# Optimization experiments

Hardware: AMD Instinct MI355X
Metric: run time of the kernel (lower is better)

## Reference

```python
import jax, jax.numpy as jnp
import numpy as np

B, T, C, H, L, V = 4, 1024, 1024, 16, 6, 32000
D = C // H
STD = 0.02


def setup_inputs() -> dict:
    key = jax.random.key(0)
    ks = jax.random.split(key, 12)
    return {
        "idx": jax.random.randint(ks[0], (B, T), 0, V),
        "tok_emb": jax.random.normal(ks[1], (V, C), jnp.float32) * STD,
        "pos_emb": jax.random.normal(ks[2], (T, C), jnp.float32) * STD,
        "qkv_w": jax.random.normal(ks[3], (L, C, 3 * C), jnp.float32) * STD,
        "attn_out_w": jax.random.normal(ks[4], (L, C, C), jnp.float32) * STD,
        "attn_out_b": jnp.zeros((L, C), jnp.float32),
        "fc1_w": jax.random.normal(ks[5], (L, C, 4 * C), jnp.float32) * STD,
        "fc1_b": jnp.zeros((L, 4 * C), jnp.float32),
        "fc2_w": jax.random.normal(ks[6], (L, 4 * C, C), jnp.float32) * STD,
        "fc2_b": jnp.zeros((L, C), jnp.float32),
        "ln1_w": jnp.ones((L, C), jnp.float32),
        "ln1_b": jnp.zeros((L, C), jnp.float32),
        "ln2_w": jnp.ones((L, C), jnp.float32),
        "ln2_b": jnp.zeros((L, C), jnp.float32),
        "lnf_w": jnp.ones((C,), jnp.float32),
        "lnf_b": jnp.zeros((C,), jnp.float32),
        "head_w": jax.random.normal(ks[7], (C, V), jnp.float32) * STD,
    }


def layernorm(x, w, b, eps=1e-5):
    mu = jnp.mean(x, axis=-1, keepdims=True)
    var = jnp.var(x, axis=-1, keepdims=True)
    return (x - mu) * jax.lax.rsqrt(var + eps) * w + b


def attention(x, qkv_w, out_w, out_b, causal_mask):
    # x: (B,T,C)
    qkv = jnp.einsum("btc,cf->btf", x, qkv_w)  # (B,T,3C)
    q, k, v = jnp.split(qkv, 3, axis=-1)
    q = q.reshape(B, T, H, D).transpose(0, 2, 1, 3)  # (B,H,T,D)
    k = k.reshape(B, T, H, D).transpose(0, 2, 1, 3)
    v = v.reshape(B, T, H, D).transpose(0, 2, 1, 3)
    scores = jnp.einsum("bhqd,bhkd->bhqk", q, k) / np.sqrt(D).astype(np.float32)
    scores = jnp.where(causal_mask, scores, -jnp.inf)
    w = jax.nn.softmax(scores, axis=-1)
    out = jnp.einsum("bhqk,bhkd->bhqd", w, v)  # (B,H,T,D)
    out = out.transpose(0, 2, 1, 3).reshape(B, T, C)
    return jnp.einsum("btc,cd->btd", out, out_w) + out_b


def reference(idx, tok_emb, pos_emb, qkv_w, attn_out_w, attn_out_b,
              fc1_w, fc1_b, fc2_w, fc2_b, ln1_w, ln1_b, ln2_w, ln2_b,
              lnf_w, lnf_b, head_w):
    causal_mask = jnp.tril(jnp.ones((T, T), dtype=bool))[None, None]  # (1,1,T,T)
    x = tok_emb[idx] + pos_emb[jnp.arange(T)][None]  # (B,T,C)
    for l in range(L):
        h = layernorm(x, ln1_w[l], ln1_b[l])
        x = x + attention(h, qkv_w[l], attn_out_w[l], attn_out_b[l], causal_mask)
        h = layernorm(x, ln2_w[l], ln2_b[l])
        h = jax.nn.relu(jnp.einsum("btc,cf->btf", h, fc1_w[l]) + fc1_b[l])
        x = x + jnp.einsum("btf,fc->btc", h, fc2_w[l]) + fc2_b[l]
    x = layernorm(x, lnf_w, lnf_b)
    logits = jnp.einsum("btc,cv->btv", x, head_w)  # (B,T,V)
    return logits
```

## Files before the change

### kernel.cpp

```cpp
#include <hip/hip_runtime.h>
#include <cstdint>
#include <cstddef>

typedef __bf16 bf16_t;
typedef __bf16 bf16x8 __attribute__((ext_vector_type(8)));
typedef float f32x4 __attribute__((ext_vector_type(4)));

#define B_ 4
#define T_ 1024
#define C_ 1024
#define H_ 16
#define L_ 6
#define V_ 32000
#define M_ (B_ * T_)

__global__ __launch_bounds__(256) void k_embed(const int* __restrict__ idx,
                                               const float* __restrict__ tok,
                                               const float* __restrict__ pos,
                                               float* __restrict__ x) {
  int row = blockIdx.x;
  int t = row & (T_ - 1);
  int id = idx[row];
  int c = threadIdx.x * 4;
  f32x4 a = *(const f32x4*)(tok + (size_t)id * C_ + c);
  f32x4 p = *(const f32x4*)(pos + (size_t)t * C_ + c);
  *(f32x4*)(x + (size_t)row * C_ + c) = a + p;
}

__global__ __launch_bounds__(256) void k_ln(const float* __restrict__ x,
                                            const float* __restrict__ w,
                                            const float* __restrict__ b,
                                            bf16_t* __restrict__ out) {
  __shared__ float red[8];
  int row = blockIdx.x;
  int tid = threadIdx.x;
  const float* xr = x + (size_t)row * C_;
  f32x4 v = *(const f32x4*)(xr + tid * 4);
  float s = v[0] + v[1] + v[2] + v[3];
  float q = v[0] * v[0] + v[1] * v[1] + v[2] * v[2] + v[3] * v[3];
#pragma unroll
  for (int off = 32; off; off >>= 1) {
    s += __shfl_xor(s, off);
    q += __shfl_xor(q, off);
  }
  int wid = tid >> 6;
  if ((tid & 63) == 0) { red[wid * 2] = s; red[wid * 2 + 1] = q; }
  __syncthreads();
  s = red[0] + red[2] + red[4] + red[6];
  q = red[1] + red[3] + red[5] + red[7];
  float mu = s * (1.f / C_);
  float var = q * (1.f / C_) - mu * mu;
  float rstd = rsqrtf(var + 1e-5f);
  f32x4 wv = *(const f32x4*)(w + tid * 4);
  f32x4 bv = *(const f32x4*)(b + tid * 4);
  bf16_t* o = out + (size_t)row * C_ + tid * 4;
#pragma unroll
  for (int j = 0; j < 4; j++) o[j] = (bf16_t)((v[j] - mu) * rstd * wv[j] + bv[j]);
}

__global__ __launch_bounds__(256) void k_transpose_bf16(const float* __restrict__ in,
                                                        bf16_t* __restrict__ out,
                                                        int K, int N) {
  __shared__ float tile[32][33];
  int n0 = blockIdx.x * 32, k0 = blockIdx.y * 32;
  int tid = threadIdx.x;
  int cr = tid >> 5, cc = tid & 31;
#pragma unroll
  for (int it = 0; it < 4; it++) {
    int r = it * 8 + cr;
    tile[r][cc] = in[(size_t)(k0 + r) * N + n0 + cc];
  }
  __syncthreads();
#pragma unroll
  for (int it = 0; it < 4; it++) {
    int r = it * 8 + cr;
    out[(size_t)(n0 + r) * K + k0 + cc] = (bf16_t)tile[cc][r];
  }
}

__global__ __launch_bounds__(256) void k_reshape_qk(const bf16_t* __restrict__ qkv,
                                                    bf16_t* __restrict__ qh,
                                                    bf16_t* __restrict__ kh) {
  int g = blockIdx.x * 256 + threadIdx.x;
  int d = g & 63;
  int t = (g >> 6) & (T_ - 1);
  int h = (g >> 16) & (H_ - 1);
  int b = g >> 20;
  size_t src = ((size_t)(b * T_ + t)) * (3 * C_) + h * 64 + d;
  qh[g] = (bf16_t)((float)qkv[src] * 0.125f);
  kh[g] = qkv[src + C_];
}

__global__ __launch_bounds__(256) void k_vtrans(const bf16_t* __restrict__ qkv,
                                                bf16_t* __restrict__ vT) {
  __shared__ bf16_t tile[64][65];
  int bh = blockIdx.x;
  int t0 = blockIdx.y * 64;
  int tid = threadIdx.x;
  int c = tid & 63, rr = tid >> 6;
  int b = bh >> 4, h = bh & (H_ - 1);
  const bf16_t* src = qkv + ((size_t)(b * T_ + t0)) * (3 * C_) + 2 * C_ + h * 64;
#pragma unroll
  for (int it = 0; it < 16; it++) {
    int r = it * 4 + rr;
    tile[r][c] = src[(size_t)r * (3 * C_) + c];
  }
  __syncthreads();
  bf16_t* dst = vT + (size_t)bh * 64 * T_ + t0;
#pragma unroll
  for (int it = 0; it < 16; it++) {
    int dr = it * 4 + rr;
    dst[(size_t)dr * T_ + c] = tile[c][dr];
  }
}

__global__ __launch_bounds__(256) void k_attn(const bf16_t* __restrict__ qh,
                                              const bf16_t* __restrict__ kh,
                                              const bf16_t* __restrict__ vT,
                                              bf16_t* __restrict__ outb) {
  __shared__ bf16_t p_lds[4][16 * 32];
  int tid = threadIdx.x, lane = tid & 63, wid = tid >> 6;
  int bh = blockIdx.x;
  int b = bh >> 4, h = bh & (H_ - 1);
  int qbase = blockIdx.y * 64 + wid * 16;
  const bf16_t* qp = qh + ((size_t)bh * T_ + qbase) * 64;
  const bf16_t* kp = kh + (size_t)bh * T_ * 64;
  const bf16_t* vp = vT + (size_t)bh * 64 * T_;
  int r = lane & 15, g = lane >> 4;

  bf16x8 qf0 = *(const bf16x8*)(qp + r * 64 + g * 8);
  bf16x8 qf1 = *(const bf16x8*)(qp + r * 64 + 32 + g * 8);

  f32x4 o[4];
  float m[4], l[4];
#pragma unroll
  for (int j = 0; j < 4; j++) { m[j] = -1e30f; l[j] = 0.f; o[j] = (f32x4){0.f, 0.f, 0.f, 0.f}; }

  int kv_end = qbase + 16;
  for (int jb = 0; jb < kv_end; jb += 32) {
    f32x4 s0 = (f32x4){0.f, 0.f, 0.f, 0.f};
    f32x4 s1 = (f32x4){0.f, 0.f, 0.f, 0.f};
    const bf16_t* kb0 = kp + (size_t)(jb + r) * 64 + g * 8;
    const bf16_t* kb1 = kb0 + 16 * 64;
    s0 = __builtin_amdgcn_mfma_f32_16x16x32_bf16(qf0, *(const bf16x8*)(kb0), s0, 0, 0, 0);
    s0 = __builtin_amdgcn_mfma_f32_16x16x32_bf16(qf1, *(const bf16x8*)(kb0 + 32), s0, 0, 0, 0);
    s1 = __builtin_amdgcn_mfma_f32_16x16x32_bf16(qf0, *(const bf16x8*)(kb1), s1, 0, 0, 0);
    s1 = __builtin_amdgcn_mfma_f32_16x16x32_bf16(qf1, *(const bf16x8*)(kb1 + 32), s1, 0, 0, 0);

    float p0[4], p1[4], fac[4];
#pragma unroll
    for (int j = 0; j < 4; j++) {
      int rowg = qbase + g * 4 + j;
      float v0 = s0[j], v1 = s1[j];
      if (jb + r > rowg) v0 = -1e30f;
      if (jb + 16 + r > rowg) v1 = -1e30f;
      float t = fmaxf(v0, v1);
      t = fmaxf(t, __shfl_xor(t, 1));
      t = fmaxf(t, __shfl_xor(t, 2));
      t = fmaxf(t, __shfl_xor(t, 4));
      t = fmaxf(t, __shfl_xor(t, 8));
      float nm = fmaxf(m[j], t);
      p0[j] = __expf(v0 - nm);
      p1[j] = __expf(v1 - nm);
      float f = __expf(m[j] - nm);
      float ts = p0[j] + p1[j];
      ts += __shfl_xor(ts, 1);
      ts += __shfl_xor(ts, 2);
      ts += __shfl_xor(ts, 4);
      ts += __shfl_xor(ts, 8);
      l[j] = l[j] * f + ts;
      m[j] = nm;
      fac[j] = f;
    }
    f32x4 fv = (f32x4){fac[0], fac[1], fac[2], fac[3]};
#pragma unroll
    for (int d = 0; d < 4; d++) o[d] *= fv;

    bf16_t* pl = p_lds[wid];
#pragma unroll
    for (int j = 0; j < 4; j++) {
      pl[(g * 4 + j) * 32 + r] = (bf16_t)p0[j];
      pl[(g * 4 + j) * 32 + 16 + r] = (bf16_t)p1[j];
    }
    bf16x8 pa = *(const bf16x8*)(pl + r * 32 + g * 8);
#pragma unroll
    for (int d = 0; d < 4; d++) {
      const bf16_t* vf = vp + (size_t)(d * 16 + r) * T_ + jb + g * 8;
      o[d] = __builtin_amdgcn_mfma_f32_16x16x32_bf16(pa, *(const bf16x8*)(vf), o[d], 0, 0, 0);
    }
  }

#pragma unroll
  for (int d = 0; d < 4; d++) {
#pragma unroll
    for (int j = 0; j < 4; j++) {
      float val = o[d][j] / l[j];
      outb[((size_t)(b * T_ + qbase + g * 4 + j)) * C_ + h * 64 + d * 16 + r] = (bf16_t)val;
    }
  }
}

__device__ __forceinline__ void gld_lds16(const bf16_t* g, bf16_t* l) {
  __builtin_amdgcn_global_load_lds((const __attribute__((address_space(1))) void*)g,
                                   (__attribute__((address_space(3))) void*)l, 16, 0, 0);
}

template <int OUTBF, int HASB, int HASRELU, int HASRES>
__global__ __launch_bounds__(256) void k_gemm(const bf16_t* __restrict__ A,
                                              const bf16_t* __restrict__ Bt,
                                              const float* __restrict__ bias,
                                              const float* resid,
                                              void* Cout, int M, int N, int K) {
  __shared__ bf16_t As[2][128 * 32];
  __shared__ bf16_t Bs[2][128 * 32];
  int tid = threadIdx.x;
  int lane = tid & 63, wid = tid >> 6;
  size_t rowBase = (size_t)blockIdx.y * 128;
  size_t colBase = (size_t)blockIdx.x * 128;

  const bf16_t* gA = A + (rowBase + (tid >> 2)) * (size_t)K + (tid & 3) * 8;
  const bf16_t* gB = Bt + (colBase + (tid >> 2)) * (size_t)K + (tid & 3) * 8;
  const size_t gStep64 = (size_t)64 * K;

  f32x4 acc[4][4];
#pragma unroll
  for (int i = 0; i < 4; i++)
#pragma unroll
    for (int j = 0; j < 4; j++) acc[i][j] = (f32x4){0.f, 0.f, 0.f, 0.f};

  int NK = K >> 5;
  {
    bf16_t* la = &As[0][0] + wid * 512;
    bf16_t* lb = &Bs[0][0] + wid * 512;
    gld_lds16(gA, la);            gld_lds16(gA + gStep64, la + 2048);
    gld_lds16(gB, lb);            gld_lds16(gB + gStep64, lb + 2048);
  }

  int wr = (wid >> 1) * 64, wc = (wid & 1) * 64;
  int r15 = lane & 15, g4 = lane >> 4;

  for (int kt = 0; kt < NK; kt++) {
    int buf = kt & 1;
    __syncthreads();
    if (kt + 1 < NK) {
      const bf16_t* ga = gA + (size_t)(kt + 1) * 32;
      const bf16_t* gb = gB + (size_t)(kt + 1) * 32;
      bf16_t* la = &As[buf ^ 1][0] + wid * 512;
      bf16_t* lb = &Bs[buf ^ 1][0] + wid * 512;
      gld_lds16(ga, la);          gld_lds16(ga + gStep64, la + 2048);
      gld_lds16(gb, lb);          gld_lds16(gb + gStep64, lb + 2048);
    }
    const bf16_t* as = &As[buf][0] + (wr + r15) * 32 + g4 * 8;
    const bf16_t* bs = &Bs[buf][0] + (wc + r15) * 32 + g4 * 8;
    bf16x8 af[4], bfr[4];
#pragma unroll
    for (int i = 0; i < 4; i++) af[i] = *(const bf16x8*)(as + i * 16 * 32);
#pragma unroll
    for (int i = 0; i < 4; i++) bfr[i] = *(const bf16x8*)(bs + i * 16 * 32);
#pragma unroll
    for (int i = 0; i < 4; i++)
#pragma unroll
      for (int j = 0; j < 4; j++)
        acc[i][j] = __builtin_amdgcn_mfma_f32_16x16x32_bf16(af[i], bfr[j], acc[i][j], 0, 0, 0);
  }

#pragma unroll
  for (int i = 0; i < 4; i++) {
    size_t row0 = rowBase + wr + i * 16 + g4 * 4;
#pragma unroll
    for (int j = 0; j < 4; j++) {
      size_t col = colBase + wc + j * 16 + r15;
      float bi = HASB ? bias[col] : 0.f;
#pragma unroll
      for (int q = 0; q < 4; q++) {
        size_t row = row0 + q;
        float v = acc[i][j][q] + bi;
        if (HASRELU) v = fmaxf(v, 0.f);
        if (HASRES) v += resid[row * (size_t)N + col];
        if (OUTBF)
          ((bf16_t*)Cout)[row * (size_t)N + col] = (bf16_t)v;
        else
          ((float*)Cout)[row * (size_t)N + col] = v;
      }
    }
  }
}

extern "C" void kernel_launch(void* const* d_in, const int* in_sizes, int n_in,
                              void* d_out, int out_size, void* d_ws, size_t ws_size,
                              hipStream_t stream) {
  (void)in_sizes; (void)n_in; (void)out_size; (void)ws_size;
  const int* idx = (const int*)d_in[0];
  const float* tok_emb = (const float*)d_in[1];
  const float* pos_emb = (const float*)d_in[2];
  const float* qkv_w = (const float*)d_in[3];
  const float* attn_out_w = (const float*)d_in[4];
  const float* attn_out_b = (const float*)d_in[5];
  const float* fc1_w = (const float*)d_in[6];
  const float* fc1_b = (const float*)d_in[7];
  const float* fc2_w = (const float*)d_in[8];
  const float* fc2_b = (const float*)d_in[9];
  const float* ln1_w = (const float*)d_in[10];
  const float* ln1_b = (const float*)d_in[11];
  const float* ln2_w = (const float*)d_in[12];
  const float* ln2_b = (const float*)d_in[13];
  const float* lnf_w = (const float*)d_in[14];
  const float* lnf_b = (const float*)d_in[15];
  const float* head_w = (const float*)d_in[16];
  float* out = (float*)d_out;

  char* wsp = (char*)d_ws;
  auto alloc = [&](size_t bytes) {
    char* p = wsp;
    wsp += (bytes + 255) & ~(size_t)255;
    return p;
  };
  float* x      = (float*)alloc((size_t)M_ * C_ * 4);
  bf16_t* hbuf  = (bf16_t*)alloc((size_t)M_ * C_ * 2);
  bf16_t* qkvb  = (bf16_t*)alloc((size_t)M_ * 3 * C_ * 2);
  bf16_t* qhb   = (bf16_t*)alloc((size_t)M_ * C_ * 2);
  bf16_t* khb   = (bf16_t*)alloc((size_t)M_ * C_ * 2);
  bf16_t* vTb   = (bf16_t*)alloc((size_t)M_ * C_ * 2);
  bf16_t* attnb = (bf16_t*)alloc((size_t)M_ * C_ * 2);
  bf16_t* midb  = (bf16_t*)alloc((size_t)M_ * 4 * C_ * 2);
  bf16_t* qkvwT = (bf16_t*)alloc((size_t)3 * C_ * C_ * 2);
  bf16_t* owT   = (bf16_t*)alloc((size_t)C_ * C_ * 2);
  bf16_t* fc1wT = (bf16_t*)alloc((size_t)4 * C_ * C_ * 2);
  bf16_t* fc2wT = (bf16_t*)alloc((size_t)4 * C_ * C_ * 2);
  bf16_t* headwT= (bf16_t*)alloc((size_t)C_ * V_ * 2);

  k_embed<<<M_, 256, 0, stream>>>(idx, tok_emb, pos_emb, x);
  k_transpose_bf16<<<dim3(V_ / 32, C_ / 32), 256, 0, stream>>>(head_w, headwT, C_, V_);

  for (int l = 0; l < L_; l++) {
    k_transpose_bf16<<<dim3(3 * C_ / 32, C_ / 32), 256, 0, stream>>>(
        qkv_w + (size_t)l * C_ * 3 * C_, qkvwT, C_, 3 * C_);
    k_transpose_bf16<<<dim3(C_ / 32, C_ / 32), 256, 0, stream>>>(
        attn_out_w + (size_t)l * C_ * C_, owT, C_, C_);
    k_transpose_bf16<<<dim3(4 * C_ / 32, C_ / 32), 256, 0, stream>>>(
        fc1_w + (size_t)l * C_ * 4 * C_, fc1wT, C_, 4 * C_);
    k_transpose_bf16<<<dim3(C_ / 32, 4 * C_ / 32), 256, 0, stream>>>(
        fc2_w + (size_t)l * 4 * C_ * C_, fc2wT, 4 * C_, C_);

    k_ln<<<M_, 256, 0, stream>>>(x, ln1_w + l * C_, ln1_b + l * C_, hbuf);
    k_gemm<1, 0, 0, 0><<<dim3(3 * C_ / 128, M_ / 128), 256, 0, stream>>>(
        hbuf, qkvwT, nullptr, nullptr, qkvb, M_, 3 * C_, C_);
    k_reshape_qk<<<(M_ * C_) / 256, 256, 0, stream>>>(qkvb, qhb, khb);
    k_vtrans<<<dim3(B_ * H_, T_ / 64), 256, 0, stream>>>(qkvb, vTb);
    k_attn<<<dim3(B_ * H_, T_ / 64), 256, 0, stream>>>(qhb, khb, vTb, attnb);
    k_gemm<0, 1, 0, 1><<<dim3(C_ / 128, M_ / 128), 256, 0, stream>>>(
        attnb, owT, attn_out_b + l * C_, x, x, M_, C_, C_);

    k_ln<<<M_, 256, 0, stream>>>(x, ln2_w + l * C_, ln2_b + l * C_, hbuf);
    k_gemm<1, 1, 1, 0><<<dim3(4 * C_ / 128, M_ / 128), 256, 0, stream>>>(
        hbuf, fc1wT, fc1_b + (size_t)l * 4 * C_, nullptr, midb, M_, 4 * C_, C_);
    k_gemm<0, 1, 0, 1><<<dim3(C_ / 128, M_ / 128), 256, 0, stream>>>(
        midb, fc2wT, fc2_b + l * C_, x, x, M_, C_, 4 * C_);
  }

  k_ln<<<M_, 256, 0, stream>>>(x, lnf_w, lnf_b, hbuf);
  k_gemm<0, 0, 0, 0><<<dim3(V_ / 128, M_ / 128), 256, 0, stream>>>(
      hbuf, headwT, nullptr, nullptr, out, M_, V_, C_);
}
```

Baseline: 2.454 ms.

## Add 256x256 tiled GEMM with swizzled LDS, XCD-aware block mapping and interleaved prefetch

Adds a new 512-thread GEMM kernel that computes 256x256 output tiles with a K-step of 64. It stages A and B into XOR-swizzled LDS through direct global-to-LDS loads, splits each K-step into four MFMA quadrants with next-tile prefetch placed between them, and maps blocks to XCDs with a swizzle to improve L2 locality. The QKV, FC1 and LM-head GEMMs switch to this kernel to get more operand reuse per byte loaded and better overlap of loads with MFMA. The trade-offs are more registers and LDS per block (64 KB), fewer blocks for occupancy, and inline asm waitcnt and barrier scheduling that is fragile.

```diff
diff --git a/kernel.cpp b/kernel.cpp
--- a/kernel.cpp
+++ b/kernel.cpp
@@ -5,6 +5,7 @@
 typedef __bf16 bf16_t;
 typedef __bf16 bf16x8 __attribute__((ext_vector_type(8)));
 typedef float f32x4 __attribute__((ext_vector_type(4)));
+typedef int i32x4 __attribute__((ext_vector_type(4)));
 
 #define B_ 4
 #define T_ 1024
@@ -204,6 +205,14 @@
   __builtin_amdgcn_global_load_lds((const __attribute__((address_space(1))) void*)g,
                                    (__attribute__((address_space(3))) void*)l, 16, 0, 0);
 }
+__device__ __forceinline__ bf16x8 lds_rd128(uint32_t addr) {
+  i32x4 d;
+  asm volatile("ds_read_b128 %0, %1" : "=v"(d) : "v"(addr));
+  return __builtin_bit_cast(bf16x8, d);
+}
+#define BAR_() __builtin_amdgcn_s_barrier()
+#define SCHED0_() __builtin_amdgcn_sched_barrier(0)
+#define WLG0_() do { asm volatile("s_waitcnt lgkmcnt(0)" ::: "memory"); SCHED0_(); } while (0)
 
 template <int OUTBF, int HASB, int HASRELU, int HASRES>
 __global__ __launch_bounds__(256) void k_gemm(const bf16_t* __restrict__ A,
@@ -275,6 +284,146 @@
       for (int q = 0; q < 4; q++) {
         size_t row = row0 + q;
         float v = acc[i][j][q] + bi;
+        if (HASRELU) v = fmaxf(v, 0.f);
+        if (HASRES) v += resid[row * (size_t)N + col];
+        if (OUTBF)
+          ((bf16_t*)Cout)[row * (size_t)N + col] = (bf16_t)v;
+        else
+          ((float*)Cout)[row * (size_t)N + col] = v;
+      }
+    }
+  }
+}
+
+#define STAGE_(q, tk, bufv)                                                           \
+  do {                                                                                \
+    const bf16_t* _ga = A + (size_t)(rowBase + (q)*64 + srow) * (size_t)K +           \
+                        (size_t)(tk)*64 + scol;                                       \
+    const bf16_t* _gb = Bt + (size_t)(colBase + (q)*64 + srow) * (size_t)K +          \
+                        (size_t)(tk)*64 + scol;                                       \
+    gld_lds16(_ga, AsF + (bufv)*16384 + (q)*4096 + w * 512);                          \
+    gld_lds16(_gb, BsF + (bufv)*16384 + (q)*4096 + w * 512);                          \
+  } while (0)
+
+#define LDA_(mh, bufv)                                                                \
+  do {                                                                                \
+    uint32_t _ab = aRd + (uint32_t)(bufv)*32768u + (mh)*8192u;                        \
+    _Pragma("unroll") for (int _m = 0; _m < 4; _m++)                                  \
+        _Pragma("unroll") for (int _k = 0; _k < 2; _k++)                              \
+            af[_m][_k] = lds_rd128(_ab + _m * 2048 + _k * 64);                        \
+  } while (0)
+
+#define LDB_(nh, bufv)                                                                \
+  do {                                                                                \
+    uint32_t _bb = bRd + (uint32_t)(bufv)*32768u + (nh)*4096u;                        \
+    _Pragma("unroll") for (int _n = 0; _n < 2; _n++)                                  \
+        _Pragma("unroll") for (int _k = 0; _k < 2; _k++)                              \
+            bfr[_n][_k] = lds_rd128(_bb + _n * 2048 + _k * 64);                       \
+  } while (0)
+
+#define MFQ_(mh, nh)                                                                  \
+  do {                                                                                \
+    __builtin_amdgcn_s_setprio(1);                                                    \
+    _Pragma("unroll") for (int _m = 0; _m < 4; _m++)                                  \
+        _Pragma("unroll") for (int _n = 0; _n < 2; _n++)                              \
+            _Pragma("unroll") for (int _k = 0; _k < 2; _k++)                          \
+                acc[(mh)*4 + _m][(nh)*2 + _n] = __builtin_amdgcn_mfma_f32_16x16x32_bf16( \
+                    af[_m][_k], bfr[_n][_k], acc[(mh)*4 + _m][(nh)*2 + _n], 0, 0, 0); \
+    __builtin_amdgcn_s_setprio(0);                                                    \
+  } while (0)
+
+template <int OUTBF, int HASB, int HASRELU, int HASRES>
+__global__ __launch_bounds__(512, 2) void k_gemm256(const bf16_t* __restrict__ A,
+                                                    const bf16_t* __restrict__ Bt,
+                                                    const float* __restrict__ bias,
+                                                    const float* resid,
+                                                    void* Cout, int M, int N, int K) {
+  __shared__ bf16_t As[2][256][64];
+  __shared__ bf16_t Bs[2][256][64];
+  bf16_t* AsF = &As[0][0][0];
+  bf16_t* BsF = &Bs[0][0][0];
+  const uint32_t asb = (uint32_t)(uintptr_t)AsF;
+  const uint32_t bsb = (uint32_t)(uintptr_t)BsF;
+
+  int tid = threadIdx.x, lane = tid & 63, w = tid >> 6;
+  int wr = w >> 2, wc = w & 3;
+  int r15 = lane & 15, g4 = lane >> 4;
+
+  int nwg = (int)gridDim.x;
+  int bid = (int)blockIdx.x;
+  int xcd = bid & 7, loc = bid >> 3;
+  int q8 = nwg >> 3, r8 = nwg & 7;
+  int swz = (xcd < r8) ? xcd * (q8 + 1) + loc : r8 * (q8 + 1) + (xcd - r8) * q8 + loc;
+  int nY = M >> 8;
+  int by = swz % nY, bx = swz / nY;
+  int rowBase = by * 256, colBase = bx * 256;
+
+  int srow = w * 8 + (lane >> 3);
+  int scol = ((lane & 7) * 8) ^ ((lane & 32) >> 1);
+
+  uint32_t xm = (uint32_t)((r15 & 4) << 3);
+  uint32_t aRd = (asb + (uint32_t)(((wr * 128 + r15) * 64 + g4 * 8) * 2)) ^ xm;
+  uint32_t bRd = (bsb + (uint32_t)(((wc * 64 + r15) * 64 + g4 * 8) * 2)) ^ xm;
+
+  f32x4 acc[8][4];
+#pragma unroll
+  for (int i = 0; i < 8; i++)
+#pragma unroll
+    for (int j = 0; j < 4; j++) acc[i][j] = (f32x4){0.f, 0.f, 0.f, 0.f};
+
+  bf16x8 af[4][2], bfr[2][2];
+
+#pragma unroll
+  for (int q = 0; q < 4; q++) STAGE_(q, 0, 0);
+
+  int NT = K >> 6;
+  for (int kt = 0; kt < NT; ++kt) {
+    int buf = kt & 1;
+    bool pf = (kt + 1 < NT);
+    if (pf) {
+      STAGE_(0, kt + 1, buf ^ 1);
+      asm volatile("s_waitcnt vmcnt(2)" ::: "memory");
+    } else {
+      asm volatile("s_waitcnt vmcnt(0)" ::: "memory");
+    }
+    BAR_();
+    SCHED0_();
+    LDA_(0, buf);
+    LDB_(0, buf);
+    WLG0_();
+    MFQ_(0, 0);
+    BAR_();
+    LDB_(1, buf);
+    if (pf) STAGE_(1, kt + 1, buf ^ 1);
+    BAR_();
+    WLG0_();
+    MFQ_(0, 1);
+    BAR_();
+    LDA_(1, buf);
+    if (pf) STAGE_(2, kt + 1, buf ^ 1);
+    BAR_();
+    WLG0_();
+    MFQ_(1, 1);
+    BAR_();
+    LDB_(0, buf);
+    if (pf) STAGE_(3, kt + 1, buf ^ 1);
+    BAR_();
+    WLG0_();
+    MFQ_(1, 0);
+    BAR_();
+  }
+
+#pragma unroll
+  for (int m = 0; m < 8; m++) {
+    size_t row0 = (size_t)rowBase + wr * 128 + m * 16 + g4 * 4;
+#pragma unroll
+    for (int n = 0; n < 4; n++) {
+      size_t col = (size_t)colBase + wc * 64 + n * 16 + r15;
+      float bi = HASB ? bias[col] : 0.f;
+#pragma unroll
+      for (int qq = 0; qq < 4; qq++) {
+        size_t row = row0 + qq;
+        float v = acc[m][n][qq] + bi;
         if (HASRELU) v = fmaxf(v, 0.f);
         if (HASRES) v += resid[row * (size_t)N + col];
         if (OUTBF)
@@ -343,7 +492,7 @@
         fc2_w + (size_t)l * 4 * C_ * C_, fc2wT, 4 * C_, C_);
 
     k_ln<<<M_, 256, 0, stream>>>(x, ln1_w + l * C_, ln1_b + l * C_, hbuf);
-    k_gemm<1, 0, 0, 0><<<dim3(3 * C_ / 128, M_ / 128), 256, 0, stream>>>(
+    k_gemm256<1, 0, 0, 0><<<dim3((3 * C_ / 256) * (M_ / 256)), 512, 0, stream>>>(
         hbuf, qkvwT, nullptr, nullptr, qkvb, M_, 3 * C_, C_);
     k_reshape_qk<<<(M_ * C_) / 256, 256, 0, stream>>>(qkvb, qhb, khb);
     k_vtrans<<<dim3(B_ * H_, T_ / 64), 256, 0, stream>>>(qkvb, vTb);
@@ -352,13 +501,13 @@
         attnb, owT, attn_out_b + l * C_, x, x, M_, C_, C_);
 
     k_ln<<<M_, 256, 0, stream>>>(x, ln2_w + l * C_, ln2_b + l * C_, hbuf);
-    k_gemm<1, 1, 1, 0><<<dim3(4 * C_ / 128, M_ / 128), 256, 0, stream>>>(
+    k_gemm256<1, 1, 1, 0><<<dim3((4 * C_ / 256) * (M_ / 256)), 512, 0, stream>>>(
         hbuf, fc1wT, fc1_b + (size_t)l * 4 * C_, nullptr, midb, M_, 4 * C_, C_);
     k_gemm<0, 1, 0, 1><<<dim3(C_ / 128, M_ / 128), 256, 0, stream>>>(
         midb, fc2wT, fc2_b + l * C_, x, x, M_, C_, 4 * C_);
   }
 
   k_ln<<<M_, 256, 0, stream>>>(x, lnf_w, lnf_b, hbuf);
-  k_gemm<0, 0, 0, 0><<<dim3(V_ / 128, M_ / 128), 256, 0, stream>>>(
+  k_gemm256<0, 0, 0, 0><<<dim3((V_ / 256) * (M_ / 256)), 512, 0, stream>>>(
       hbuf, headwT, nullptr, nullptr, out, M_, V_, C_);
 }
```

Measured after the change: 2.369 ms. -3.4%, faster.
